# Performance work log

Hardware: AMD Instinct MI355X
Metric: run time of the kernel (lower is better)

Reference implementation:

```python
import jax, jax.numpy as jnp
import numpy as np

N_NODES = 100000
N_EDGES = 1600000
N_FEAT = 128
HIDDEN = 64
N_CLASSES = 40


def _gcn_layer(x, W, b, src, dst, w, n):
    # Linear transform first (as in torch_geometric GCNConv), then normalized aggregation.
    h = x @ W  # [N, out]
    # Add self-loops with weight 1.
    loop = jnp.arange(n, dtype=src.dtype)
    src_f = jnp.concatenate([src, loop])
    dst_f = jnp.concatenate([dst, loop])
    w_f = jnp.concatenate([w, jnp.ones((n,), dtype=w.dtype)])
    # Symmetric normalization deg^-1/2 * w * deg^-1/2 (deg computed at dst).
    deg = jax.ops.segment_sum(w_f, dst_f, num_segments=n)
    dinv = jnp.where(deg > 0, jax.lax.rsqrt(deg), 0.0)
    norm = dinv[src_f] * w_f * dinv[dst_f]  # [E+N]
    # Gather-scale-scatter aggregation.
    out = jax.ops.segment_sum(norm[:, None] * h[src_f], dst_f, num_segments=n)
    return out + b


def setup_inputs() -> dict:
    key = jax.random.key(0)
    ks = jax.random.split(key, 7)
    x = jax.random.normal(ks[0], (N_NODES, N_FEAT), dtype=jnp.float32)
    edge_index = jax.random.randint(ks[1], (2, N_EDGES), 0, N_NODES, dtype=jnp.int64)
    edge_weight = jax.random.uniform(ks[2], (N_EDGES,), dtype=jnp.float32)
    # Glorot-ish init for the two GCNConv linear weights.
    W1 = jax.random.normal(ks[3], (N_FEAT, HIDDEN), dtype=jnp.float32) * (1.0 / np.sqrt(N_FEAT))
    b1 = jnp.zeros((HIDDEN,), dtype=jnp.float32)
    W2 = jax.random.normal(ks[4], (HIDDEN, N_CLASSES), dtype=jnp.float32) * (1.0 / np.sqrt(HIDDEN))
    b2 = jnp.zeros((N_CLASSES,), dtype=jnp.float32)
    return {"x": x, "edge_index": edge_index, "edge_weight": edge_weight,
            "W1": W1, "b1": b1, "W2": W2, "b2": b2}


def reference(x, edge_index, edge_weight, W1, b1, W2, b2):
    n = x.shape[0]
    src, dst = edge_index[0], edge_index[1]
    h = jax.nn.relu(_gcn_layer(x, W1, b1, src, dst, edge_weight, n))
    # F.dropout(training=self.training): inference mode -> identity.
    h = _gcn_layer(h, W2, b2, src, dst, edge_weight, n)
    return jax.nn.log_softmax(h, axis=1)
```

## Files before the change

kernel.cpp:

```cpp
#include <hip/hip_runtime.h>
#include <hip/hip_bf16.h>
#include <math.h>


#define NFEAT 128
#define HID 64
#define NCLS 40
#define PB 512
#define BSH 7
#define NBUK_MAX 1024

static __device__ __forceinline__ unsigned short f2bf(float f) {
    unsigned u = __float_as_uint(f);
    unsigned r = (u + 0x7fffu + ((u >> 16) & 1u)) >> 16;
    return (unsigned short)r;
}
static __device__ __forceinline__ float bf2f(unsigned short b) {
    return __uint_as_float(((unsigned)b) << 16);
}

__global__ __launch_bounds__(256) void k_hist(const int* __restrict__ dst,
                                              int* __restrict__ ghist,
                                              int e, int nbuk, int epb) {
    __shared__ int hist[NBUK_MAX];
    for (int j = threadIdx.x; j < nbuk; j += 256) hist[j] = 0;
    __syncthreads();
    int b = blockIdx.x;
    int lo = b * epb, hi = min(lo + epb, e);
    for (int i = lo + threadIdx.x; i < hi; i += 256)
        atomicAdd(&hist[dst[i] >> BSH], 1);
    __syncthreads();
    for (int j = threadIdx.x; j < nbuk; j += 256) ghist[j * PB + b] = hist[j];
}

__global__ __launch_bounds__(256) void k_colscan(int* __restrict__ ghist,
                                                 int* __restrict__ buktot, int nbuk) {
    __shared__ int s[256];
    int k = blockIdx.x, t = threadIdx.x;
    int* col = ghist + k * PB;
    int v0 = col[2 * t], v1 = col[2 * t + 1];
    int sum = v0 + v1;
    s[t] = sum; __syncthreads();
    for (int off = 1; off < 256; off <<= 1) {
        int x = (t >= off) ? s[t - off] : 0;
        __syncthreads();
        s[t] += x;
        __syncthreads();
    }
    int excl = s[t] - sum;
    col[2 * t] = excl;
    col[2 * t + 1] = excl + v0;
    if (t == 255) buktot[k] = s[255];
}

__global__ __launch_bounds__(256) void k_bukscan(const int* __restrict__ buktot,
                                                 int* __restrict__ bukstart,
                                                 int* __restrict__ rowptr,
                                                 int nbuk, int n, int e) {
    __shared__ int s[256];
    int t = threadIdx.x;
    int v[4]; int sum = 0;
#pragma unroll
    for (int j = 0; j < 4; j++) { int idx = t * 4 + j; v[j] = (idx < nbuk) ? buktot[idx] : 0; sum += v[j]; }
    s[t] = sum; __syncthreads();
    for (int off = 1; off < 256; off <<= 1) {
        int x = (t >= off) ? s[t - off] : 0;
        __syncthreads();
        s[t] += x;
        __syncthreads();
    }
    int excl = s[t] - sum;
#pragma unroll
    for (int j = 0; j < 4; j++) { int idx = t * 4 + j; if (idx < nbuk) bukstart[idx] = excl; excl += v[j]; }
    if (t == 255) bukstart[nbuk] = s[255];
    if (t == 0) rowptr[n] = e;
}

__global__ __launch_bounds__(256) void k_bucketize(const int* __restrict__ src,
                                                   const int* __restrict__ dst,
                                                   const float* __restrict__ w,
                                                   const int* __restrict__ ghist,
                                                   const int* __restrict__ bukstart,
                                                   unsigned long long* __restrict__ sedge,
                                                   int e, int nbuk, int epb) {
    __shared__ int loff[NBUK_MAX];
    int b = blockIdx.x;
    for (int j = threadIdx.x; j < nbuk; j += 256) loff[j] = bukstart[j] + ghist[j * PB + b];
    __syncthreads();
    int lo = b * epb, hi = min(lo + epb, e);
    for (int i = lo + threadIdx.x; i < hi; i += 256) {
        int d = dst[i], s = src[i];
        int k = d >> BSH;
        int pos = atomicAdd(&loff[k], 1);
        unsigned long long rec = ((unsigned long long)__float_as_uint(w[i]) << 32)
                               | ((unsigned)(d & 127) << 17) | (unsigned)s;
        sedge[pos] = rec;
    }
}

__global__ __launch_bounds__(256) void k_bucket_csr(const unsigned long long* __restrict__ sedge,
                                                    const int* __restrict__ bukstart,
                                                    int* __restrict__ rowptr,
                                                    float* __restrict__ dinv,
                                                    int2* __restrict__ edges, int n) {
    __shared__ int cnt[128]; __shared__ float wsum[128];
    __shared__ int fill[128]; __shared__ int rloc[128];
    int k = blockIdx.x, t = threadIdx.x;
    int base = k << BSH;
    int nloc = n - base; if (nloc > 128) nloc = 128;
    if (t < 128) { cnt[t] = 0; fill[t] = 0; wsum[t] = 1.0f; }
    __syncthreads();
    int lo = bukstart[k], hi = bukstart[k + 1];
    for (int p = lo + t; p < hi; p += 256) {
        unsigned long long r = sedge[p];
        int dloc = (int)((r >> 17) & 127);
        atomicAdd(&cnt[dloc], 1);
        atomicAdd(&wsum[dloc], __uint_as_float((unsigned)(r >> 32)));
    }
    __syncthreads();
    if (t < 128) rloc[t] = cnt[t];
    __syncthreads();
    for (int off = 1; off < 128; off <<= 1) {
        int x = 0;
        if (t < 128 && t >= off) x = rloc[t - off];
        __syncthreads();
        if (t < 128) rloc[t] += x;
        __syncthreads();
    }
    if (t < 128) {
        int excl = rloc[t] - cnt[t];
        rloc[t] = excl;
        if (t < nloc) {
            rowptr[base + t] = lo + excl;
            dinv[base + t] = rsqrtf(wsum[t]);
        }
    }
    __syncthreads();
    for (int p = lo + t; p < hi; p += 256) {
        unsigned long long r = sedge[p];
        int dloc = (int)((r >> 17) & 127);
        int srcn = (int)(r & 0x1ffff);
        int pos = lo + rloc[dloc] + atomicAdd(&fill[dloc], 1);
        edges[pos] = make_int2((dloc << 17) | srcn, (int)(unsigned)(r >> 32));
    }
}

__global__ __launch_bounds__(256) void k_norm(const int* __restrict__ bukstart,
                                              const float* __restrict__ dinv,
                                              int2* __restrict__ edges, int n) {
    int k = blockIdx.x;
    int base = k << BSH;
    int lo = bukstart[k], hi = bukstart[k + 1];
    for (int p = lo + threadIdx.x; p < hi; p += 256) {
        int2 rec = edges[p];
        int dloc = rec.x >> 17, srcn = rec.x & 0x1ffff;
        float v = __int_as_float(rec.y) * dinv[srcn] * dinv[base + dloc];
        edges[p] = make_int2(srcn, __float_as_int(v));
    }
}

__global__ __launch_bounds__(256) void k_gemm1(const float* __restrict__ x,
                                               const float* __restrict__ W1,
                                               unsigned short* __restrict__ h1, int n) {
    __shared__ float xs[64 * 65];
    int t = threadIdx.x;
    int lane = t & 63;
    int wid = __builtin_amdgcn_readfirstlane(t >> 6);
    int base = blockIdx.x * 64;
    int nrows = n - base; if (nrows > 64) nrows = 64;
    const float4* xg = reinterpret_cast<const float4*>(x + (size_t)base * NFEAT);
    float acc[16];
#pragma unroll
    for (int c = 0; c < 16; c++) acc[c] = 0.f;
#pragma unroll
    for (int h = 0; h < 2; h++) {
        for (int j = t; j < nrows * 16; j += 256) {
            int row = j >> 4, k4 = j & 15;
            float4 v = xg[row * 32 + h * 16 + k4];
            xs[(4 * k4 + 0) * 65 + row] = v.x;
            xs[(4 * k4 + 1) * 65 + row] = v.y;
            xs[(4 * k4 + 2) * 65 + row] = v.z;
            xs[(4 * k4 + 3) * 65 + row] = v.w;
        }
        __syncthreads();
        const float* wb = W1 + (size_t)(h * 64) * HID + wid * 16;
#pragma unroll 4
        for (int k = 0; k < 64; k++) {
            float xv = xs[k * 65 + lane];
            const float* wk = wb + k * HID;
#pragma unroll
            for (int c = 0; c < 16; c++) acc[c] = fmaf(wk[c], xv, acc[c]);
        }
        __syncthreads();
    }
    if (lane < nrows) {
        unsigned pk[8];
#pragma unroll
        for (int j = 0; j < 8; j++)
            pk[j] = (unsigned)f2bf(acc[2 * j]) | ((unsigned)f2bf(acc[2 * j + 1]) << 16);
        uint4* hp = reinterpret_cast<uint4*>(h1 + (size_t)(base + lane) * HID + wid * 16);
        hp[0] = make_uint4(pk[0], pk[1], pk[2], pk[3]);
        hp[1] = make_uint4(pk[4], pk[5], pk[6], pk[7]);
    }
}

__global__ __launch_bounds__(256) void k_gemm2(const float* __restrict__ y,
                                               const float* __restrict__ W2,
                                               unsigned short* __restrict__ h2, int n) {
    __shared__ float ys[HID * 65];
    int t = threadIdx.x;
    int lane = t & 63;
    int wid = __builtin_amdgcn_readfirstlane(t >> 6);
    int base = blockIdx.x * 64;
    int nrows = n - base; if (nrows > 64) nrows = 64;
    const float4* yg = reinterpret_cast<const float4*>(y + (size_t)base * HID);
    for (int j = t; j < nrows * 16; j += 256) {
        int row = j >> 4, k4 = j & 15;
        float4 v = yg[j];
        ys[(4 * k4 + 0) * 65 + row] = v.x;
        ys[(4 * k4 + 1) * 65 + row] = v.y;
        ys[(4 * k4 + 2) * 65 + row] = v.z;
        ys[(4 * k4 + 3) * 65 + row] = v.w;
    }
    __syncthreads();
    const float* wb = W2 + wid * 10;
    float acc[10];
#pragma unroll
    for (int c = 0; c < 10; c++) acc[c] = 0.f;
#pragma unroll 4
    for (int k = 0; k < HID; k++) {
        float yv = ys[k * 65 + lane];
        const float* wk = wb + k * NCLS;
#pragma unroll
        for (int c = 0; c < 10; c++) acc[c] = fmaf(wk[c], yv, acc[c]);
    }
    if (lane < nrows) {
        unsigned* hp = reinterpret_cast<unsigned*>(h2 + (size_t)(base + lane) * NCLS + wid * 10);
#pragma unroll
        for (int j = 0; j < 5; j++)
            hp[j] = (unsigned)f2bf(acc[2 * j]) | ((unsigned)f2bf(acc[2 * j + 1]) << 16);
    }
}

__global__ __launch_bounds__(256) void k_agg1(const unsigned short* __restrict__ h1,
                                              const int* __restrict__ rowptr,
                                              const int2* __restrict__ edges,
                                              const float* __restrict__ dinv,
                                              const float* __restrict__ b1,
                                              float* __restrict__ y, int n) {
    int lane = threadIdx.x & 63;
    int wid = threadIdx.x >> 6;
    for (int node = blockIdx.x * 4 + wid; node < n; node += gridDim.x * 4) {
        int i = __builtin_amdgcn_readfirstlane(node);
        float di = dinv[i];
        float a0 = di * di * bf2f(h1[(size_t)i * HID + lane]);
        float a1 = 0.f, a2 = 0.f, a3 = 0.f, a4 = 0.f, a5 = 0.f, a6 = 0.f, a7 = 0.f;
        int s = rowptr[i], e = rowptr[i + 1];
        int p = s;
        for (; p + 8 <= e; p += 8) {
            int2 e0 = edges[p], e1 = edges[p + 1], e2 = edges[p + 2], e3 = edges[p + 3];
            int2 e4 = edges[p + 4], e5 = edges[p + 5], e6 = edges[p + 6], e7 = edges[p + 7];
            a0 = fmaf(__int_as_float(e0.y), bf2f(h1[(size_t)e0.x * HID + lane]), a0);
            a1 = fmaf(__int_as_float(e1.y), bf2f(h1[(size_t)e1.x * HID + lane]), a1);
            a2 = fmaf(__int_as_float(e2.y), bf2f(h1[(size_t)e2.x * HID + lane]), a2);
            a3 = fmaf(__int_as_float(e3.y), bf2f(h1[(size_t)e3.x * HID + lane]), a3);
            a4 = fmaf(__int_as_float(e4.y), bf2f(h1[(size_t)e4.x * HID + lane]), a4);
            a5 = fmaf(__int_as_float(e5.y), bf2f(h1[(size_t)e5.x * HID + lane]), a5);
            a6 = fmaf(__int_as_float(e6.y), bf2f(h1[(size_t)e6.x * HID + lane]), a6);
            a7 = fmaf(__int_as_float(e7.y), bf2f(h1[(size_t)e7.x * HID + lane]), a7);
        }
        for (; p + 4 <= e; p += 4) {
            int2 e0 = edges[p], e1 = edges[p + 1], e2 = edges[p + 2], e3 = edges[p + 3];
            a0 = fmaf(__int_as_float(e0.y), bf2f(h1[(size_t)e0.x * HID + lane]), a0);
            a1 = fmaf(__int_as_float(e1.y), bf2f(h1[(size_t)e1.x * HID + lane]), a1);
            a2 = fmaf(__int_as_float(e2.y), bf2f(h1[(size_t)e2.x * HID + lane]), a2);
            a3 = fmaf(__int_as_float(e3.y), bf2f(h1[(size_t)e3.x * HID + lane]), a3);
        }
        for (; p < e; p++) {
            int2 e0 = edges[p];
            a0 = fmaf(__int_as_float(e0.y), bf2f(h1[(size_t)e0.x * HID + lane]), a0);
        }
        float acc = ((a0 + a1) + (a2 + a3)) + ((a4 + a5) + (a6 + a7)) + b1[lane];
        y[(size_t)i * HID + lane] = fmaxf(acc, 0.f);
    }
}

__global__ __launch_bounds__(256) void k_agg2(const unsigned short* __restrict__ h2,
                                              const int* __restrict__ rowptr,
                                              const int2* __restrict__ edges,
                                              const float* __restrict__ dinv,
                                              const float* __restrict__ b2,
                                              float* __restrict__ out, int n) {
    int lane = threadIdx.x & 63;
    int wid = threadIdx.x >> 6;
    for (int node = blockIdx.x * 4 + wid; node < n; node += gridDim.x * 4) {
        int i = __builtin_amdgcn_readfirstlane(node);
        float di = dinv[i];
        int c = lane < NCLS ? lane : 0;
        float a0 = di * di * bf2f(h2[(size_t)i * NCLS + c]);
        float a1 = 0.f, a2 = 0.f, a3 = 0.f, a4 = 0.f, a5 = 0.f, a6 = 0.f, a7 = 0.f;
        int s = rowptr[i], e = rowptr[i + 1];
        int p = s;
        for (; p + 8 <= e; p += 8) {
            int2 e0 = edges[p], e1 = edges[p + 1], e2 = edges[p + 2], e3 = edges[p + 3];
            int2 e4 = edges[p + 4], e5 = edges[p + 5], e6 = edges[p + 6], e7 = edges[p + 7];
            a0 = fmaf(__int_as_float(e0.y), bf2f(h2[(size_t)e0.x * NCLS + c]), a0);
            a1 = fmaf(__int_as_float(e1.y), bf2f(h2[(size_t)e1.x * NCLS + c]), a1);
            a2 = fmaf(__int_as_float(e2.y), bf2f(h2[(size_t)e2.x * NCLS + c]), a2);
            a3 = fmaf(__int_as_float(e3.y), bf2f(h2[(size_t)e3.x * NCLS + c]), a3);
            a4 = fmaf(__int_as_float(e4.y), bf2f(h2[(size_t)e4.x * NCLS + c]), a4);
            a5 = fmaf(__int_as_float(e5.y), bf2f(h2[(size_t)e5.x * NCLS + c]), a5);
            a6 = fmaf(__int_as_float(e6.y), bf2f(h2[(size_t)e6.x * NCLS + c]), a6);
            a7 = fmaf(__int_as_float(e7.y), bf2f(h2[(size_t)e7.x * NCLS + c]), a7);
        }
        for (; p + 4 <= e; p += 4) {
            int2 e0 = edges[p], e1 = edges[p + 1], e2 = edges[p + 2], e3 = edges[p + 3];
            a0 = fmaf(__int_as_float(e0.y), bf2f(h2[(size_t)e0.x * NCLS + c]), a0);
            a1 = fmaf(__int_as_float(e1.y), bf2f(h2[(size_t)e1.x * NCLS + c]), a1);
            a2 = fmaf(__int_as_float(e2.y), bf2f(h2[(size_t)e2.x * NCLS + c]), a2);
            a3 = fmaf(__int_as_float(e3.y), bf2f(h2[(size_t)e3.x * NCLS + c]), a3);
        }
        for (; p < e; p++) {
            int2 e0 = edges[p];
            a0 = fmaf(__int_as_float(e0.y), bf2f(h2[(size_t)e0.x * NCLS + c]), a0);
        }
        float acc = ((a0 + a1) + (a2 + a3)) + ((a4 + a5) + (a6 + a7)) + b2[c];
        float z = lane < NCLS ? acc : -INFINITY;
        float m = z;
#pragma unroll
        for (int off = 32; off > 0; off >>= 1) m = fmaxf(m, __shfl_xor(m, off));
        float ex = lane < NCLS ? expf(z - m) : 0.f;
        float ssum = ex;
#pragma unroll
        for (int off = 32; off > 0; off >>= 1) ssum += __shfl_xor(ssum, off);
        if (lane < NCLS) out[(size_t)i * NCLS + lane] = z - m - logf(ssum);
    }
}


extern "C" void kernel_launch(void* const* d_in, const int* in_sizes, int n_in,
                              void* d_out, int out_size, void* d_ws, size_t ws_size,
                              hipStream_t stream) {
    const float* x = (const float*)d_in[0];
    const int* edge_index = (const int*)d_in[1];
    const float* ew = (const float*)d_in[2];
    const float* W1 = (const float*)d_in[3];
    const float* b1 = (const float*)d_in[4];
    const float* W2 = (const float*)d_in[5];
    const float* b2 = (const float*)d_in[6];
    float* out = (float*)d_out;

    const int N = in_sizes[0] / NFEAT;
    const int E = in_sizes[2];
    const int* src = edge_index;
    const int* dst = edge_index + E;

    const int NBUK = (N + 127) >> BSH;
    const int EPB = (E + PB - 1) / PB;

    char* ws = (char*)d_ws;
    size_t off = 0;
    auto alloc = [&](size_t bytes) { void* p = ws + off; off = (off + bytes + 255) & ~(size_t)255; return p; };
    int*   ghist    = (int*)alloc((size_t)NBUK_MAX * PB * 4);
    int*   buktot   = (int*)alloc(4096);
    int*   bukstart = (int*)alloc(4096 + 4);
    int*   rowptr   = (int*)alloc((size_t)(N + 1) * 4);
    float* dinv     = (float*)alloc((size_t)N * 4);
    int2*  edges    = (int2*)alloc((size_t)E * 8);
    float* y        = (float*)alloc((size_t)N * HID * 4);
    unsigned long long* sedge = (unsigned long long*)alloc((size_t)E * 8);
    unsigned short* h1 = (unsigned short*)sedge;
    unsigned short* h2 = h1;

    k_hist<<<PB, 256, 0, stream>>>(dst, ghist, E, NBUK, EPB);
    k_colscan<<<NBUK, 256, 0, stream>>>(ghist, buktot, NBUK);
    k_bukscan<<<1, 256, 0, stream>>>(buktot, bukstart, rowptr, NBUK, N, E);
    k_bucketize<<<PB, 256, 0, stream>>>(src, dst, ew, ghist, bukstart, sedge, E, NBUK, EPB);
    k_bucket_csr<<<NBUK, 256, 0, stream>>>(sedge, bukstart, rowptr, dinv, edges, N);
    k_norm<<<NBUK, 256, 0, stream>>>(bukstart, dinv, edges, N);
    k_gemm1<<<(N + 63) / 64, 256, 0, stream>>>(x, W1, h1, N);
    k_agg1<<<(N + 3) / 4, 256, 0, stream>>>(h1, rowptr, edges, dinv, b1, y, N);
    k_gemm2<<<(N + 63) / 64, 256, 0, stream>>>(y, W2, h2, N);
    k_agg2<<<(N + 3) / 4, 256, 0, stream>>>(h2, rowptr, edges, dinv, b2, out, N);
}
```

Before: 306.4 us.

## Reorder second GCN layer to aggregate before linear transform, fuse log-softmax

Layer 2 now aggregates the 64-wide hidden features (stored as bf16) over edges first, then applies W2, bias and log-softmax in one per-tile kernel. This removes the separate h2 intermediate and computes log-softmax per row from shared memory instead of wave shuffles. It also halves the y buffer by storing it in bf16. The trade-off is that edge gathers now fetch 64 features per edge instead of 40, increasing gather traffic, and y loses precision.

```diff
diff --git a/kernel.cpp b/kernel.cpp
--- a/kernel.cpp
+++ b/kernel.cpp
@@ -204,50 +204,12 @@
     }
 }
 
-__global__ __launch_bounds__(256) void k_gemm2(const float* __restrict__ y,
-                                               const float* __restrict__ W2,
-                                               unsigned short* __restrict__ h2, int n) {
-    __shared__ float ys[HID * 65];
-    int t = threadIdx.x;
-    int lane = t & 63;
-    int wid = __builtin_amdgcn_readfirstlane(t >> 6);
-    int base = blockIdx.x * 64;
-    int nrows = n - base; if (nrows > 64) nrows = 64;
-    const float4* yg = reinterpret_cast<const float4*>(y + (size_t)base * HID);
-    for (int j = t; j < nrows * 16; j += 256) {
-        int row = j >> 4, k4 = j & 15;
-        float4 v = yg[j];
-        ys[(4 * k4 + 0) * 65 + row] = v.x;
-        ys[(4 * k4 + 1) * 65 + row] = v.y;
-        ys[(4 * k4 + 2) * 65 + row] = v.z;
-        ys[(4 * k4 + 3) * 65 + row] = v.w;
-    }
-    __syncthreads();
-    const float* wb = W2 + wid * 10;
-    float acc[10];
-#pragma unroll
-    for (int c = 0; c < 10; c++) acc[c] = 0.f;
-#pragma unroll 4
-    for (int k = 0; k < HID; k++) {
-        float yv = ys[k * 65 + lane];
-        const float* wk = wb + k * NCLS;
-#pragma unroll
-        for (int c = 0; c < 10; c++) acc[c] = fmaf(wk[c], yv, acc[c]);
-    }
-    if (lane < nrows) {
-        unsigned* hp = reinterpret_cast<unsigned*>(h2 + (size_t)(base + lane) * NCLS + wid * 10);
-#pragma unroll
-        for (int j = 0; j < 5; j++)
-            hp[j] = (unsigned)f2bf(acc[2 * j]) | ((unsigned)f2bf(acc[2 * j + 1]) << 16);
-    }
-}
-
 __global__ __launch_bounds__(256) void k_agg1(const unsigned short* __restrict__ h1,
                                               const int* __restrict__ rowptr,
                                               const int2* __restrict__ edges,
                                               const float* __restrict__ dinv,
                                               const float* __restrict__ b1,
-                                              float* __restrict__ y, int n) {
+                                              unsigned short* __restrict__ y, int n) {
     int lane = threadIdx.x & 63;
     int wid = threadIdx.x >> 6;
     for (int node = blockIdx.x * 4 + wid; node < n; node += gridDim.x * 4) {
@@ -281,59 +243,100 @@
             a0 = fmaf(__int_as_float(e0.y), bf2f(h1[(size_t)e0.x * HID + lane]), a0);
         }
         float acc = ((a0 + a1) + (a2 + a3)) + ((a4 + a5) + (a6 + a7)) + b1[lane];
-        y[(size_t)i * HID + lane] = fmaxf(acc, 0.f);
-    }
-}
-
-__global__ __launch_bounds__(256) void k_agg2(const unsigned short* __restrict__ h2,
+        y[(size_t)i * HID + lane] = f2bf(fmaxf(acc, 0.f));
+    }
+}
+
+__global__ __launch_bounds__(256) void k_aggz(const unsigned short* __restrict__ y,
                                               const int* __restrict__ rowptr,
                                               const int2* __restrict__ edges,
                                               const float* __restrict__ dinv,
-                                              const float* __restrict__ b2,
-                                              float* __restrict__ out, int n) {
+                                              float* __restrict__ z, int n) {
     int lane = threadIdx.x & 63;
     int wid = threadIdx.x >> 6;
     for (int node = blockIdx.x * 4 + wid; node < n; node += gridDim.x * 4) {
         int i = __builtin_amdgcn_readfirstlane(node);
         float di = dinv[i];
-        int c = lane < NCLS ? lane : 0;
-        float a0 = di * di * bf2f(h2[(size_t)i * NCLS + c]);
+        float a0 = di * di * bf2f(y[(size_t)i * HID + lane]);
         float a1 = 0.f, a2 = 0.f, a3 = 0.f, a4 = 0.f, a5 = 0.f, a6 = 0.f, a7 = 0.f;
         int s = rowptr[i], e = rowptr[i + 1];
         int p = s;
         for (; p + 8 <= e; p += 8) {
             int2 e0 = edges[p], e1 = edges[p + 1], e2 = edges[p + 2], e3 = edges[p + 3];
             int2 e4 = edges[p + 4], e5 = edges[p + 5], e6 = edges[p + 6], e7 = edges[p + 7];
-            a0 = fmaf(__int_as_float(e0.y), bf2f(h2[(size_t)e0.x * NCLS + c]), a0);
-            a1 = fmaf(__int_as_float(e1.y), bf2f(h2[(size_t)e1.x * NCLS + c]), a1);
-            a2 = fmaf(__int_as_float(e2.y), bf2f(h2[(size_t)e2.x * NCLS + c]), a2);
-            a3 = fmaf(__int_as_float(e3.y), bf2f(h2[(size_t)e3.x * NCLS + c]), a3);
-            a4 = fmaf(__int_as_float(e4.y), bf2f(h2[(size_t)e4.x * NCLS + c]), a4);
-            a5 = fmaf(__int_as_float(e5.y), bf2f(h2[(size_t)e5.x * NCLS + c]), a5);
-            a6 = fmaf(__int_as_float(e6.y), bf2f(h2[(size_t)e6.x * NCLS + c]), a6);
-            a7 = fmaf(__int_as_float(e7.y), bf2f(h2[(size_t)e7.x * NCLS + c]), a7);
+            a0 = fmaf(__int_as_float(e0.y), bf2f(y[(size_t)e0.x * HID + lane]), a0);
+            a1 = fmaf(__int_as_float(e1.y), bf2f(y[(size_t)e1.x * HID + lane]), a1);
+            a2 = fmaf(__int_as_float(e2.y), bf2f(y[(size_t)e2.x * HID + lane]), a2);
+            a3 = fmaf(__int_as_float(e3.y), bf2f(y[(size_t)e3.x * HID + lane]), a3);
+            a4 = fmaf(__int_as_float(e4.y), bf2f(y[(size_t)e4.x * HID + lane]), a4);
+            a5 = fmaf(__int_as_float(e5.y), bf2f(y[(size_t)e5.x * HID + lane]), a5);
+            a6 = fmaf(__int_as_float(e6.y), bf2f(y[(size_t)e6.x * HID + lane]), a6);
+            a7 = fmaf(__int_as_float(e7.y), bf2f(y[(size_t)e7.x * HID + lane]), a7);
         }
         for (; p + 4 <= e; p += 4) {
             int2 e0 = edges[p], e1 = edges[p + 1], e2 = edges[p + 2], e3 = edges[p + 3];
-            a0 = fmaf(__int_as_float(e0.y), bf2f(h2[(size_t)e0.x * NCLS + c]), a0);
-            a1 = fmaf(__int_as_float(e1.y), bf2f(h2[(size_t)e1.x * NCLS + c]), a1);
-            a2 = fmaf(__int_as_float(e2.y), bf2f(h2[(size_t)e2.x * NCLS + c]), a2);
-            a3 = fmaf(__int_as_float(e3.y), bf2f(h2[(size_t)e3.x * NCLS + c]), a3);
+            a0 = fmaf(__int_as_float(e0.y), bf2f(y[(size_t)e0.x * HID + lane]), a0);
+            a1 = fmaf(__int_as_float(e1.y), bf2f(y[(size_t)e1.x * HID + lane]), a1);
+            a2 = fmaf(__int_as_float(e2.y), bf2f(y[(size_t)e2.x * HID + lane]), a2);
+            a3 = fmaf(__int_as_float(e3.y), bf2f(y[(size_t)e3.x * HID + lane]), a3);
         }
         for (; p < e; p++) {
             int2 e0 = edges[p];
-            a0 = fmaf(__int_as_float(e0.y), bf2f(h2[(size_t)e0.x * NCLS + c]), a0);
-        }
-        float acc = ((a0 + a1) + (a2 + a3)) + ((a4 + a5) + (a6 + a7)) + b2[c];
-        float z = lane < NCLS ? acc : -INFINITY;
-        float m = z;
-#pragma unroll
-        for (int off = 32; off > 0; off >>= 1) m = fmaxf(m, __shfl_xor(m, off));
-        float ex = lane < NCLS ? expf(z - m) : 0.f;
-        float ssum = ex;
-#pragma unroll
-        for (int off = 32; off > 0; off >>= 1) ssum += __shfl_xor(ssum, off);
-        if (lane < NCLS) out[(size_t)i * NCLS + lane] = z - m - logf(ssum);
+            a0 = fmaf(__int_as_float(e0.y), bf2f(y[(size_t)e0.x * HID + lane]), a0);
+        }
+        float acc = ((a0 + a1) + (a2 + a3)) + ((a4 + a5) + (a6 + a7));
+        z[(size_t)i * HID + lane] = acc;
+    }
+}
+
+__global__ __launch_bounds__(256) void k_gemm2s(const float* __restrict__ z,
+                                                const float* __restrict__ W2,
+                                                const float* __restrict__ b2,
+                                                float* __restrict__ out, int n) {
+    __shared__ float ys[HID * 65];
+    __shared__ float zs[64 * 41];
+    int t = threadIdx.x;
+    int lane = t & 63;
+    int wid = __builtin_amdgcn_readfirstlane(t >> 6);
+    int base = blockIdx.x * 64;
+    int nrows = n - base; if (nrows > 64) nrows = 64;
+    const float4* yg = reinterpret_cast<const float4*>(z + (size_t)base * HID);
+    for (int j = t; j < nrows * 16; j += 256) {
+        int row = j >> 4, k4 = j & 15;
+        float4 v = yg[j];
+        ys[(4 * k4 + 0) * 65 + row] = v.x;
+        ys[(4 * k4 + 1) * 65 + row] = v.y;
+        ys[(4 * k4 + 2) * 65 + row] = v.z;
+        ys[(4 * k4 + 3) * 65 + row] = v.w;
+    }
+    __syncthreads();
+    const float* wb = W2 + wid * 10;
+    float acc[10];
+#pragma unroll
+    for (int c = 0; c < 10; c++) acc[c] = b2[wid * 10 + c];
+#pragma unroll 4
+    for (int k = 0; k < HID; k++) {
+        float yv = ys[k * 65 + lane];
+        const float* wk = wb + k * NCLS;
+#pragma unroll
+        for (int c = 0; c < 10; c++) acc[c] = fmaf(wk[c], yv, acc[c]);
+    }
+#pragma unroll
+    for (int c = 0; c < 10; c++) zs[lane * 41 + wid * 10 + c] = acc[c];
+    __syncthreads();
+    if (lane < nrows) {
+        const float* zr = zs + lane * 41;
+        float m = zr[0];
+#pragma unroll
+        for (int j = 1; j < NCLS; j++) m = fmaxf(m, zr[j]);
+        float sum = 0.f;
+#pragma unroll
+        for (int j = 0; j < NCLS; j++) sum += expf(zr[j] - m);
+        float lse = m + logf(sum);
+        float2* op = reinterpret_cast<float2*>(out + (size_t)(base + lane) * NCLS + wid * 10);
+#pragma unroll
+        for (int j = 0; j < 5; j++)
+            op[j] = make_float2(acc[2 * j] - lse, acc[2 * j + 1] - lse);
     }
 }
 
@@ -367,10 +370,11 @@
     int*   rowptr   = (int*)alloc((size_t)(N + 1) * 4);
     float* dinv     = (float*)alloc((size_t)N * 4);
     int2*  edges    = (int2*)alloc((size_t)E * 8);
-    float* y        = (float*)alloc((size_t)N * HID * 4);
-    unsigned long long* sedge = (unsigned long long*)alloc((size_t)E * 8);
-    unsigned short* h1 = (unsigned short*)sedge;
-    unsigned short* h2 = h1;
+    unsigned short* ybuf = (unsigned short*)alloc((size_t)N * HID * 2);
+    void* uni = alloc((size_t)N * HID * 4);
+    unsigned long long* sedge = (unsigned long long*)uni;
+    unsigned short* h1 = (unsigned short*)uni;
+    float* z = (float*)uni;
 
     k_hist<<<PB, 256, 0, stream>>>(dst, ghist, E, NBUK, EPB);
     k_colscan<<<NBUK, 256, 0, stream>>>(ghist, buktot, NBUK);
@@ -379,7 +383,7 @@
     k_bucket_csr<<<NBUK, 256, 0, stream>>>(sedge, bukstart, rowptr, dinv, edges, N);
     k_norm<<<NBUK, 256, 0, stream>>>(bukstart, dinv, edges, N);
     k_gemm1<<<(N + 63) / 64, 256, 0, stream>>>(x, W1, h1, N);
-    k_agg1<<<(N + 3) / 4, 256, 0, stream>>>(h1, rowptr, edges, dinv, b1, y, N);
-    k_gemm2<<<(N + 63) / 64, 256, 0, stream>>>(y, W2, h2, N);
-    k_agg2<<<(N + 3) / 4, 256, 0, stream>>>(h2, rowptr, edges, dinv, b2, out, N);
-}
+    k_agg1<<<(N + 3) / 4, 256, 0, stream>>>(h1, rowptr, edges, dinv, b1, ybuf, N);
+    k_aggz<<<(N + 3) / 4, 256, 0, stream>>>(ybuf, rowptr, edges, dinv, z, N);
+    k_gemm2s<<<(N + 63) / 64, 256, 0, stream>>>(z, W2, b2, out, N);
+}
```

After: 314.0 us. 2.5% more time.
